# Performance work log

Hardware: AMD Instinct MI355X
Metric: run time of the kernel (lower is better)

The kernel has to match this reference:

```python
import jax, jax.numpy as jnp
import numpy as np

N, D, E, R = 1024, 128, 32768, 32  # nodes, hidden, edges, rank-net width
EPS = 1e-5


def setup_inputs() -> dict:
    key = jax.random.key(0)
    ks = jax.random.split(key, 16)
    s = 0.02
    f32 = jnp.float32
    return {
        "x": jax.random.normal(ks[0], (N, D), f32),
        "edge_index": jax.random.randint(ks[1], (2, E), 0, N),
        # SAGEConv (mean aggr): lin_l (with bias) on aggregated neighbors, lin_r (no bias) on root
        "W_l": jax.random.normal(ks[2], (D, D), f32) * s,
        "b_l": jnp.zeros((D,), f32),
        "W_r": jax.random.normal(ks[3], (D, D), f32) * s,
        # rank_net: Linear(D,32) -> ReLU -> Linear(32,1)
        "W1": jax.random.normal(ks[4], (R, D), f32) * s,
        "b1": jnp.zeros((R,), f32),
        "W2": jax.random.normal(ks[5], (1, R), f32) * s,
        "b2": jnp.zeros((1,), f32),
        # MambaBlock params
        "Wp": jax.random.normal(ks[6], (4 * D, D), f32) * s,   # proj, no bias
        "A": jax.random.normal(ks[7], (1, 1, D), f32) * s,
        "Bp": jax.random.normal(ks[8], (1, D, 1), f32) * s,
        "Dp": jnp.ones((1,), f32),
        "Wd": jax.random.normal(ks[9], (D, D), f32) * s,       # delta linear
        "bd": jnp.zeros((D,), f32),
    }


def reference(x, edge_index, W_l, b_l, W_r, W1, b1, W2, b2, Wp, A, Bp, Dp, Wd, bd):
    src, dst = edge_index[0], edge_index[1]

    # ---- SAGEConv (mean) + residual + GELU ----
    agg = jax.ops.segment_sum(x[src], dst, num_segments=N)                      # [N,D]
    cnt = jax.ops.segment_sum(jnp.ones((E,), x.dtype), dst, num_segments=N)    # [N]
    mean = agg / jnp.maximum(cnt, 1.0)[:, None]
    x_gnn = mean @ W_l.T + b_l + x @ W_r.T + x
    x_gnn = jax.nn.gelu(x_gnn, approximate=False)

    # ---- dynamic sort: rank_net score + degree, argsort descending ----
    scores = (jax.nn.relu(x_gnn @ W1.T + b1) @ W2.T + b2)[:, 0]                # [N]
    deg = jnp.zeros((N,), x.dtype).at[src].add(1.0).at[dst].add(1.0)
    scores = scores + deg
    idx = jnp.argsort(-scores)          # soft_rank is monotone -> same ordering as raw scores
    xs = x_gnn[idx]                      # [N,D]

    # ---- MambaBlock on the sorted node sequence (batch=1, seq_len=N, hidden=D) ----
    proj = xs @ Wp.T                                    # [N,4D]
    delta, _Bs, Cs, residual = jnp.split(proj, 4, axis=-1)  # split B is unused (as in source)
    delta = jax.nn.softplus(delta @ Wd.T + bd)          # [N,D]
    Av = A[0, 0]                                        # [D]
    Bv = Bp[0, :, 0]                                    # [D]
    dA = (jnp.exp(delta * Av) * Bv).T                   # [D,N]  einsum('blh,bhn->bhl') with n=1
    dB = jnp.cumsum(delta * Bv, axis=0).T               # [D,N]  cumsum over seq, n=1
    u = xs.T                                            # [D,N]
    Ct = Cs.T                                           # [D,N]
    kernel = jnp.einsum('hl,hn->hnl', dA, u) + dB[:, None, :]   # [D,N,N] large intermediate
    y = jnp.einsum('hnl,hn->hl', kernel, Ct).T                  # [N,D]
    out = y + residual * Dp[0]

    # F.layer_norm without affine params
    mu = out.mean(-1, keepdims=True)
    var = out.var(-1, keepdims=True)
    out = (out - mu) / jnp.sqrt(var + EPS)

    inv = jnp.argsort(idx)
    return x + out[inv]
```

## Files before the change

kernel.cpp:

```cpp
#include <hip/hip_runtime.h>

namespace {
constexpr int N   = 1024;
constexpr int D   = 128;
constexpr int E   = 32768;
constexpr int CAP = 128;

using short8  = __attribute__((ext_vector_type(8))) short;
using floatx4 = __attribute__((ext_vector_type(4))) float;

__device__ __forceinline__ unsigned short f2bf(float f){
  unsigned int u = __float_as_uint(f);
  unsigned int r = (u + 0x7FFFu + ((u >> 16) & 1u)) >> 16;
  return (unsigned short)r;
}
__device__ __forceinline__ float bf2f(unsigned short b){
  return __uint_as_float(((unsigned int)b) << 16);
}
__device__ __forceinline__ short8 ldfrag(const float* p){
  float4 a = *(const float4*)p;
  float4 b = *(const float4*)(p + 4);
  short8 r;
  r[0]=(short)f2bf(a.x); r[1]=(short)f2bf(a.y); r[2]=(short)f2bf(a.z); r[3]=(short)f2bf(a.w);
  r[4]=(short)f2bf(b.x); r[5]=(short)f2bf(b.y); r[6]=(short)f2bf(b.z); r[7]=(short)f2bf(b.w);
  return r;
}

__global__ __launch_bounds__(1024) void k_zero(int* __restrict__ cnt, int* __restrict__ srcdeg){
  int t = threadIdx.x;
  cnt[t] = 0;
  srcdeg[t] = 0;
}

__global__ void k_edges(const int* __restrict__ ei, int* __restrict__ cnt,
                        int* __restrict__ srcdeg, int* __restrict__ bucket){
  int e = blockIdx.x*256 + threadIdx.x;
  if(e < E){
    int s = ei[e], d = ei[E+e];
    int slot = atomicAdd(&cnt[d], 1);
    if(slot < CAP) bucket[d*CAP + slot] = s;
    atomicAdd(&srcdeg[s], 1);
  }
}

__global__ __launch_bounds__(256) void k_mean(const float* __restrict__ x,
    const int* __restrict__ cnt, const int* __restrict__ bucket,
    float* __restrict__ mean, float* __restrict__ s1, float* __restrict__ s2){
  int t = threadIdx.x;
  if(blockIdx.x == 0 && t < D){ s1[t] = 0.f; s2[t] = 0.f; }
  int f = t & 127, hh = t >> 7;
  int n = blockIdx.x*2 + hh;
  int c0 = cnt[n];
  int c = c0 < CAP ? c0 : CAP;
  const int* bk = bucket + n*CAP;
  float a0=0.f, a1=0.f, a2=0.f, a3=0.f;
  int j = 0;
  for(; j+3 < c; j += 4){
    int i0=bk[j], i1=bk[j+1], i2=bk[j+2], i3=bk[j+3];
    a0 += x[i0*D+f]; a1 += x[i1*D+f]; a2 += x[i2*D+f]; a3 += x[i3*D+f];
  }
  for(; j < c; ++j) a0 += x[bk[j]*D+f];
  mean[n*D + f] = (a0+a1+a2+a3) / (float)(c0 > 1 ? c0 : 1);
}


__global__ __launch_bounds__(64) void k_g1(
    const float* __restrict__ x, const float* __restrict__ mean,
    const float* __restrict__ Wl, const float* __restrict__ bl,
    const float* __restrict__ Wr, unsigned short* __restrict__ xg)
{
  int bid = blockIdx.x;
  int strip = bid >> 3, ct = bid & 7;
  int l = threadIdx.x, lr = l & 15, lg = l >> 4;
  int r0 = strip*16;

  const float* mrow = mean + (size_t)(r0+lr)*D + lg*8;
  const float* xrow = x    + (size_t)(r0+lr)*D + lg*8;
  short8 am[4], ax[4];
  #pragma unroll
  for(int s = 0; s < 4; ++s){ am[s] = ldfrag(mrow + s*32); ax[s] = ldfrag(xrow + s*32); }

  const float* wl = Wl + (size_t)(ct*16+lr)*D + lg*8;
  const float* wr = Wr + (size_t)(ct*16+lr)*D + lg*8;
  floatx4 acc = {0.f,0.f,0.f,0.f};
  #pragma unroll
  for(int s = 0; s < 4; ++s) acc = __builtin_amdgcn_mfma_f32_16x16x32_bf16(am[s], ldfrag(wl + s*32), acc, 0,0,0);
  #pragma unroll
  for(int s = 0; s < 4; ++s) acc = __builtin_amdgcn_mfma_f32_16x16x32_bf16(ax[s], ldfrag(wr + s*32), acc, 0,0,0);

  int col = ct*16 + lr;
  float blv = bl[col];
  #pragma unroll
  for(int rg = 0; rg < 4; ++rg){
    int row = lg*4 + rg;
    float v = acc[rg] + blv + x[(size_t)(r0+row)*D + col];
    float g = 0.5f*v*(1.0f + erff(v*0.7071067811865475f));
    xg[(size_t)(r0+row)*D + col] = f2bf(g);
  }
}

__global__ __launch_bounds__(64) void k_g2(
    const unsigned short* __restrict__ xg,
    const float* __restrict__ Wp, const float* __restrict__ W1,
    const float* __restrict__ b1, const float* __restrict__ W2,
    const float* __restrict__ b2,
    const int* __restrict__ cnt, const int* __restrict__ srcdeg,
    unsigned short* __restrict__ dr, float* __restrict__ res,
    float* __restrict__ s1, float* __restrict__ s2,
    float* __restrict__ scores)
{
  int bid = blockIdx.x;
  int strip = bid / 25, tt = bid - strip*25;
  int l = threadIdx.x, lr = l & 15, lg = l >> 4;
  int r0 = strip*16;

  const unsigned short* agp = xg + (size_t)(r0+lr)*D + lg*8;
  short8 ag[4];
  #pragma unroll
  for(int s = 0; s < 4; ++s) ag[s] = *(const short8*)(agp + s*32);

  if(tt < 24){
    int seg = tt >> 3, ctl = tt & 7;
    int wrow = (seg == 0) ? ctl*16 : (seg == 1) ? (2*D + ctl*16) : (3*D + ctl*16);
    const float* bp = Wp + (size_t)(wrow + lr)*D + lg*8;
    floatx4 acc = {0.f,0.f,0.f,0.f};
    #pragma unroll
    for(int s = 0; s < 4; ++s) acc = __builtin_amdgcn_mfma_f32_16x16x32_bf16(ag[s], ldfrag(bp + s*32), acc, 0,0,0);
    if(seg == 0){
      int col = ctl*16 + lr;
      #pragma unroll
      for(int rg = 0; rg < 4; ++rg) dr[(size_t)(r0+lg*4+rg)*D + col] = f2bf(acc[rg]);
    } else if(seg == 1){
      int h = ctl*16 + lr;
      float ls1 = 0.f, ls2 = 0.f;
      #pragma unroll
      for(int rg = 0; rg < 4; ++rg){
        float c = acc[rg];
        ls1 += bf2f(xg[(size_t)(r0+lg*4+rg)*D + h]) * c;
        ls2 += c;
      }
      ls1 += __shfl_xor(ls1, 16); ls1 += __shfl_xor(ls1, 32);
      ls2 += __shfl_xor(ls2, 16); ls2 += __shfl_xor(ls2, 32);
      if(lg == 0){ atomicAdd(&s1[h], ls1); atomicAdd(&s2[h], ls2); }
    } else {
      int col = ctl*16 + lr;
      #pragma unroll
      for(int rg = 0; rg < 4; ++rg) res[(size_t)(r0+lg*4+rg)*D + col] = acc[rg];
    }
  } else {
    floatx4 sa0 = {0.f,0.f,0.f,0.f}, sa1 = {0.f,0.f,0.f,0.f};
    const float* w10 = W1 + (size_t)(lr)*D + lg*8;
    const float* w11 = W1 + (size_t)(16+lr)*D + lg*8;
    #pragma unroll
    for(int s = 0; s < 4; ++s){
      sa0 = __builtin_amdgcn_mfma_f32_16x16x32_bf16(ag[s], ldfrag(w10 + s*32), sa0, 0,0,0);
      sa1 = __builtin_amdgcn_mfma_f32_16x16x32_bf16(ag[s], ldfrag(w11 + s*32), sa1, 0,0,0);
    }
    float b10 = b1[lr], b11 = b1[16+lr];
    float w20 = W2[lr], w21 = W2[16+lr];
    #pragma unroll
    for(int rg = 0; rg < 4; ++rg){
      float v = fmaxf(sa0[rg] + b10, 0.f)*w20 + fmaxf(sa1[rg] + b11, 0.f)*w21;
      v += __shfl_xor(v, 1); v += __shfl_xor(v, 2);
      v += __shfl_xor(v, 4); v += __shfl_xor(v, 8);
      if(lr == 0){
        int row = r0 + lg*4 + rg;
        scores[row] = v + b2[0] + (float)(cnt[row] + srcdeg[row]);
      }
    }
  }
}

__global__ __launch_bounds__(64) void k_g3rank(
    const unsigned short* __restrict__ dr,
    const float* __restrict__ Wd, const float* __restrict__ bd,
    float* __restrict__ delta,
    const float* __restrict__ scores, int* __restrict__ sidx)
{
  int bid = blockIdx.x;
  int l = threadIdx.x;
  if(bid < 512){
    int strip = bid >> 3, ct = bid & 7;
    int lr = l & 15, lg = l >> 4;
    int r0 = strip*16;
    const unsigned short* adp = dr + (size_t)(r0+lr)*D + lg*8;
    short8 ad[4];
    #pragma unroll
    for(int s = 0; s < 4; ++s) ad[s] = *(const short8*)(adp + s*32);
    const float* wd = Wd + (size_t)(ct*16+lr)*D + lg*8;
    floatx4 acc = {0.f,0.f,0.f,0.f};
    #pragma unroll
    for(int s = 0; s < 4; ++s) acc = __builtin_amdgcn_mfma_f32_16x16x32_bf16(ad[s], ldfrag(wd + s*32), acc, 0,0,0);
    int col = ct*16 + lr;
    float bdv = bd[col];
    #pragma unroll
    for(int rg = 0; rg < 4; ++rg){
      float d2 = acc[rg] + bdv;
      float sp = (d2 > 20.f) ? d2 : log1pf(expf(d2));
      delta[(size_t)(r0+lg*4+rg)*D + col] = sp;
    }
  } else {
    int i = bid - 512;
    float si = scores[i];
    int c = 0;
    #pragma unroll
    for(int ch = 0; ch < 4; ++ch){
      float4 sj = *(const float4*)&scores[l*4 + ch*256];
      #pragma unroll
      for(int k = 0; k < 4; ++k){
        int j = l*4 + ch*256 + k;
        float s = (k==0)?sj.x:(k==1)?sj.y:(k==2)?sj.z:sj.w;
        c += (s > si || (s == si && j < i)) ? 1 : 0;
      }
    }
    #pragma unroll
    for(int m = 1; m < 64; m <<= 1) c += __shfl_xor(c, m);
    if(l == 0) sidx[c] = i;
  }
}

__global__ __launch_bounds__(1024) void k_cumsum(const float* __restrict__ delta,
     const int* __restrict__ sidx, const float* __restrict__ Bp, float* __restrict__ pfx){
  int t = threadIdx.x, h0 = blockIdx.x*4;
  int i = sidx[t];
  float4 dv = *(const float4*)&delta[i*D + h0];
  float4 bv = *(const float4*)&Bp[h0];
  float v0 = dv.x*bv.x, v1 = dv.y*bv.y, v2 = dv.z*bv.z, v3 = dv.w*bv.w;
  int lane = t & 63, w = t >> 6;
  #pragma unroll
  for(int o2 = 1; o2 < 64; o2 <<= 1){
    float n0 = __shfl_up(v0, o2, 64), n1 = __shfl_up(v1, o2, 64);
    float n2 = __shfl_up(v2, o2, 64), n3 = __shfl_up(v3, o2, 64);
    if(lane >= o2){ v0 += n0; v1 += n1; v2 += n2; v3 += n3; }
  }
  __shared__ float4 wsum[16];
  if(lane == 63) wsum[w] = make_float4(v0, v1, v2, v3);
  __syncthreads();
  float p0=0.f, p1=0.f, p2=0.f, p3=0.f;
  #pragma unroll
  for(int i2 = 0; i2 < 16; ++i2){
    float4 sv = wsum[i2];
    if(i2 < w){ p0 += sv.x; p1 += sv.y; p2 += sv.z; p3 += sv.w; }
  }
  float4 outv; outv.x = v0+p0; outv.y = v1+p1; outv.z = v2+p2; outv.w = v3+p3;
  *(float4*)&pfx[t*D + h0] = outv;
}

__global__ __launch_bounds__(128) void k_final(
    const float* __restrict__ delta, const float* __restrict__ res,
    const float* __restrict__ pfx, const int* __restrict__ sidx,
    const float* __restrict__ s1, const float* __restrict__ s2,
    const float* __restrict__ A, const float* __restrict__ Bp,
    const float* __restrict__ Dp, const float* __restrict__ x,
    float* __restrict__ out){
  int l = blockIdx.x, h = threadIdx.x;
  int i = sidx[l];
  float dlt = delta[i*D + h];
  float dAv = expf(dlt * A[h]) * Bp[h];
  float o = dAv * s1[h] + pfx[l*D + h] * s2[h] + res[i*D + h] * Dp[0];
  __shared__ float sm1[2], sm2[2];
  float v = o;
  v += __shfl_down(v, 32); v += __shfl_down(v, 16); v += __shfl_down(v, 8);
  v += __shfl_down(v, 4);  v += __shfl_down(v, 2);  v += __shfl_down(v, 1);
  int wid = h >> 6, lane = h & 63;
  if(lane == 0) sm1[wid] = v;
  __syncthreads();
  float mean = (sm1[0] + sm1[1]) * (1.0f/(float)D);
  float cdev = o - mean;
  float cv = cdev * cdev;
  cv += __shfl_down(cv, 32); cv += __shfl_down(cv, 16); cv += __shfl_down(cv, 8);
  cv += __shfl_down(cv, 4);  cv += __shfl_down(cv, 2);  cv += __shfl_down(cv, 1);
  if(lane == 0) sm2[wid] = cv;
  __syncthreads();
  float var = (sm2[0] + sm2[1]) * (1.0f/(float)D);
  float nrm = cdev * rsqrtf(var + 1e-5f);
  out[i*D + h] = x[i*D + h] + nrm;
}

}

extern "C" void kernel_launch(void* const* d_in, const int* in_sizes, int n_in,
                              void* d_out, int out_size, void* d_ws, size_t ws_size,
                              hipStream_t stream){
  const float* x   = (const float*)d_in[0];
  const int*   ei  = (const int*)d_in[1];
  const float* Wl  = (const float*)d_in[2];
  const float* bl  = (const float*)d_in[3];
  const float* Wr  = (const float*)d_in[4];
  const float* W1  = (const float*)d_in[5];
  const float* b1  = (const float*)d_in[6];
  const float* W2  = (const float*)d_in[7];
  const float* b2  = (const float*)d_in[8];
  const float* Wp  = (const float*)d_in[9];
  const float* A   = (const float*)d_in[10];
  const float* Bp  = (const float*)d_in[11];
  const float* Dp  = (const float*)d_in[12];
  const float* Wd  = (const float*)d_in[13];
  const float* bd  = (const float*)d_in[14];

  char* ws = (char*)d_ws;
  size_t o = 0;
  auto alloc = [&](size_t bytes)->char*{
    char* p = ws + o;
    o = (o + bytes + 255) & ~(size_t)255;
    return p;
  };
  float* s1     = (float*)alloc(D*4);
  float* s2     = (float*)alloc(D*4);
  int*   cnt    = (int*)  alloc(N*4);
  int*   srcdeg = (int*)  alloc(N*4);
  int*   bucket = (int*)  alloc((size_t)N*CAP*4);
  float* meanb  = (float*)alloc((size_t)N*D*4);
  unsigned short* xg = (unsigned short*)alloc((size_t)N*D*2);
  unsigned short* dr = (unsigned short*)alloc((size_t)N*D*2);
  float* scores = (float*)alloc(N*4);
  int*   sidx   = (int*)  alloc(N*4);
  float* delta  = (float*)alloc((size_t)N*D*4);
  float* res    = (float*)alloc((size_t)N*D*4);
  float* pfx    = (float*)alloc((size_t)N*D*4);
  (void)ws_size; (void)in_sizes; (void)n_in; (void)out_size;

  k_zero  <<<1, 1024, 0, stream>>>(cnt, srcdeg);
  k_edges <<<(E+255)/256, 256, 0, stream>>>(ei, cnt, srcdeg, bucket);
  k_mean  <<<N/2, 256, 0, stream>>>(x, cnt, bucket, meanb, s1, s2);
  k_g1    <<<64*8, 64, 0, stream>>>(x, meanb, Wl, bl, Wr, xg);
  k_g2    <<<64*25, 64, 0, stream>>>(xg, Wp, W1, b1, W2, b2, cnt, srcdeg, dr, res, s1, s2, scores);
  k_g3rank<<<512+1024, 64, 0, stream>>>(dr, Wd, bd, delta, scores, sidx);
  k_cumsum<<<D/4, 1024, 0, stream>>>(delta, sidx, Bp, pfx);
  k_final <<<N, 128, 0, stream>>>(delta, res, pfx, sidx, s1, s2, A, Bp, Dp, x, (float*)d_out);
}
```

Before: 51.63 us.

## Pre-convert weights to bf16 once and split neighbor gather across two halves

The zero-init kernel now also converts Wl, Wr, Wd, W1 and Wp to bf16 buffers. The GEMM kernels load short8 fragments directly instead of loading fp32 and converting per tile, which removes repeated conversion work and halves weight bytes. The mean kernel now uses one block per node, with each half of the block summing half the neighbor list and the two partials combined through shared memory. This adds a conversion pass each call and a block sync in k_mean.

```diff
diff --git a/kernel.cpp b/kernel.cpp
--- a/kernel.cpp
+++ b/kernel.cpp
@@ -26,10 +26,32 @@
   return r;
 }
 
-__global__ __launch_bounds__(1024) void k_zero(int* __restrict__ cnt, int* __restrict__ srcdeg){
-  int t = threadIdx.x;
-  cnt[t] = 0;
-  srcdeg[t] = 0;
+__global__ __launch_bounds__(256) void k_zero(
+    int* __restrict__ cnt, int* __restrict__ srcdeg,
+    const float* __restrict__ Wl, const float* __restrict__ Wr,
+    const float* __restrict__ Wd, const float* __restrict__ W1,
+    const float* __restrict__ Wp,
+    unsigned short* __restrict__ wlb, unsigned short* __restrict__ wrb,
+    unsigned short* __restrict__ wdb, unsigned short* __restrict__ w1b,
+    unsigned short* __restrict__ wpb)
+{
+  int t = threadIdx.x, b = blockIdx.x;
+  if(b == 0){
+    ((int4*)cnt)[t]    = make_int4(0,0,0,0);
+    ((int4*)srcdeg)[t] = make_int4(0,0,0,0);
+    return;
+  }
+  const int T = 16384*3 + 4096 + 65536;
+  int stride = 128*256;
+  for(int i = (b-1)*256 + t; i < T; i += stride){
+    float v; unsigned short* dst;
+    if(i < 16384){            v = Wl[i];          dst = &wlb[i]; }
+    else if(i < 32768){       v = Wr[i-16384];    dst = &wrb[i-16384]; }
+    else if(i < 49152){       v = Wd[i-32768];    dst = &wdb[i-32768]; }
+    else if(i < 53248){       v = W1[i-49152];    dst = &w1b[i-49152]; }
+    else {                    v = Wp[i-53248];    dst = &wpb[i-53248]; }
+    *dst = f2bf(v);
+  }
 }
 
 __global__ void k_edges(const int* __restrict__ ei, int* __restrict__ cnt,
@@ -46,28 +68,34 @@
 __global__ __launch_bounds__(256) void k_mean(const float* __restrict__ x,
     const int* __restrict__ cnt, const int* __restrict__ bucket,
     float* __restrict__ mean, float* __restrict__ s1, float* __restrict__ s2){
+  __shared__ float sacc[128];
   int t = threadIdx.x;
-  if(blockIdx.x == 0 && t < D){ s1[t] = 0.f; s2[t] = 0.f; }
-  int f = t & 127, hh = t >> 7;
-  int n = blockIdx.x*2 + hh;
+  int n = blockIdx.x;
+  if(n == 0 && t < D){ s1[t] = 0.f; s2[t] = 0.f; }
+  int f = t & 127, j2 = t >> 7;
   int c0 = cnt[n];
   int c = c0 < CAP ? c0 : CAP;
   const int* bk = bucket + n*CAP;
+  int ch = (c + 1) >> 1;
+  int beg = j2 * ch, end = beg + ch < c ? beg + ch : c;
   float a0=0.f, a1=0.f, a2=0.f, a3=0.f;
-  int j = 0;
-  for(; j+3 < c; j += 4){
+  int j = beg;
+  for(; j+3 < end; j += 4){
     int i0=bk[j], i1=bk[j+1], i2=bk[j+2], i3=bk[j+3];
     a0 += x[i0*D+f]; a1 += x[i1*D+f]; a2 += x[i2*D+f]; a3 += x[i3*D+f];
   }
-  for(; j < c; ++j) a0 += x[bk[j]*D+f];
-  mean[n*D + f] = (a0+a1+a2+a3) / (float)(c0 > 1 ? c0 : 1);
+  for(; j < end; ++j) a0 += x[bk[j]*D+f];
+  float part = (a0+a1)+(a2+a3);
+  if(j2 == 1) sacc[f] = part;
+  __syncthreads();
+  if(j2 == 0) mean[n*D + f] = (part + sacc[f]) / (float)(c0 > 1 ? c0 : 1);
 }
 
 
 __global__ __launch_bounds__(64) void k_g1(
     const float* __restrict__ x, const float* __restrict__ mean,
-    const float* __restrict__ Wl, const float* __restrict__ bl,
-    const float* __restrict__ Wr, unsigned short* __restrict__ xg)
+    const unsigned short* __restrict__ wlb, const float* __restrict__ bl,
+    const unsigned short* __restrict__ wrb, unsigned short* __restrict__ xg)
 {
   int bid = blockIdx.x;
   int strip = bid >> 3, ct = bid & 7;
@@ -80,13 +108,13 @@
   #pragma unroll
   for(int s = 0; s < 4; ++s){ am[s] = ldfrag(mrow + s*32); ax[s] = ldfrag(xrow + s*32); }
 
-  const float* wl = Wl + (size_t)(ct*16+lr)*D + lg*8;
-  const float* wr = Wr + (size_t)(ct*16+lr)*D + lg*8;
+  const unsigned short* wl = wlb + (size_t)(ct*16+lr)*D + lg*8;
+  const unsigned short* wr = wrb + (size_t)(ct*16+lr)*D + lg*8;
   floatx4 acc = {0.f,0.f,0.f,0.f};
   #pragma unroll
-  for(int s = 0; s < 4; ++s) acc = __builtin_amdgcn_mfma_f32_16x16x32_bf16(am[s], ldfrag(wl + s*32), acc, 0,0,0);
-  #pragma unroll
-  for(int s = 0; s < 4; ++s) acc = __builtin_amdgcn_mfma_f32_16x16x32_bf16(ax[s], ldfrag(wr + s*32), acc, 0,0,0);
+  for(int s = 0; s < 4; ++s) acc = __builtin_amdgcn_mfma_f32_16x16x32_bf16(am[s], *(const short8*)(wl + s*32), acc, 0,0,0);
+  #pragma unroll
+  for(int s = 0; s < 4; ++s) acc = __builtin_amdgcn_mfma_f32_16x16x32_bf16(ax[s], *(const short8*)(wr + s*32), acc, 0,0,0);
 
   int col = ct*16 + lr;
   float blv = bl[col];
@@ -101,7 +129,7 @@
 
 __global__ __launch_bounds__(64) void k_g2(
     const unsigned short* __restrict__ xg,
-    const float* __restrict__ Wp, const float* __restrict__ W1,
+    const unsigned short* __restrict__ wpb, const unsigned short* __restrict__ w1b,
     const float* __restrict__ b1, const float* __restrict__ W2,
     const float* __restrict__ b2,
     const int* __restrict__ cnt, const int* __restrict__ srcdeg,
@@ -122,10 +150,10 @@
   if(tt < 24){
     int seg = tt >> 3, ctl = tt & 7;
     int wrow = (seg == 0) ? ctl*16 : (seg == 1) ? (2*D + ctl*16) : (3*D + ctl*16);
-    const float* bp = Wp + (size_t)(wrow + lr)*D + lg*8;
+    const unsigned short* bp = wpb + (size_t)(wrow + lr)*D + lg*8;
     floatx4 acc = {0.f,0.f,0.f,0.f};
     #pragma unroll
-    for(int s = 0; s < 4; ++s) acc = __builtin_amdgcn_mfma_f32_16x16x32_bf16(ag[s], ldfrag(bp + s*32), acc, 0,0,0);
+    for(int s = 0; s < 4; ++s) acc = __builtin_amdgcn_mfma_f32_16x16x32_bf16(ag[s], *(const short8*)(bp + s*32), acc, 0,0,0);
     if(seg == 0){
       int col = ctl*16 + lr;
       #pragma unroll
@@ -149,12 +177,12 @@
     }
   } else {
     floatx4 sa0 = {0.f,0.f,0.f,0.f}, sa1 = {0.f,0.f,0.f,0.f};
-    const float* w10 = W1 + (size_t)(lr)*D + lg*8;
-    const float* w11 = W1 + (size_t)(16+lr)*D + lg*8;
+    const unsigned short* w10 = w1b + (size_t)(lr)*D + lg*8;
+    const unsigned short* w11 = w1b + (size_t)(16+lr)*D + lg*8;
     #pragma unroll
     for(int s = 0; s < 4; ++s){
-      sa0 = __builtin_amdgcn_mfma_f32_16x16x32_bf16(ag[s], ldfrag(w10 + s*32), sa0, 0,0,0);
-      sa1 = __builtin_amdgcn_mfma_f32_16x16x32_bf16(ag[s], ldfrag(w11 + s*32), sa1, 0,0,0);
+      sa0 = __builtin_amdgcn_mfma_f32_16x16x32_bf16(ag[s], *(const short8*)(w10 + s*32), sa0, 0,0,0);
+      sa1 = __builtin_amdgcn_mfma_f32_16x16x32_bf16(ag[s], *(const short8*)(w11 + s*32), sa1, 0,0,0);
     }
     float b10 = b1[lr], b11 = b1[16+lr];
     float w20 = W2[lr], w21 = W2[16+lr];
@@ -173,7 +201,7 @@
 
 __global__ __launch_bounds__(64) void k_g3rank(
     const unsigned short* __restrict__ dr,
-    const float* __restrict__ Wd, const float* __restrict__ bd,
+    const unsigned short* __restrict__ wdb, const float* __restrict__ bd,
     float* __restrict__ delta,
     const float* __restrict__ scores, int* __restrict__ sidx)
 {
@@ -187,10 +215,10 @@
     short8 ad[4];
     #pragma unroll
     for(int s = 0; s < 4; ++s) ad[s] = *(const short8*)(adp + s*32);
-    const float* wd = Wd + (size_t)(ct*16+lr)*D + lg*8;
+    const unsigned short* wd = wdb + (size_t)(ct*16+lr)*D + lg*8;
     floatx4 acc = {0.f,0.f,0.f,0.f};
     #pragma unroll
-    for(int s = 0; s < 4; ++s) acc = __builtin_amdgcn_mfma_f32_16x16x32_bf16(ad[s], ldfrag(wd + s*32), acc, 0,0,0);
+    for(int s = 0; s < 4; ++s) acc = __builtin_amdgcn_mfma_f32_16x16x32_bf16(ad[s], *(const short8*)(wd + s*32), acc, 0,0,0);
     int col = ct*16 + lr;
     float bdv = bd[col];
     #pragma unroll
@@ -311,8 +339,13 @@
   int*   srcdeg = (int*)  alloc(N*4);
   int*   bucket = (int*)  alloc((size_t)N*CAP*4);
   float* meanb  = (float*)alloc((size_t)N*D*4);
-  unsigned short* xg = (unsigned short*)alloc((size_t)N*D*2);
-  unsigned short* dr = (unsigned short*)alloc((size_t)N*D*2);
+  unsigned short* xg  = (unsigned short*)alloc((size_t)N*D*2);
+  unsigned short* dr  = (unsigned short*)alloc((size_t)N*D*2);
+  unsigned short* wlb = (unsigned short*)alloc((size_t)D*D*2);
+  unsigned short* wrb = (unsigned short*)alloc((size_t)D*D*2);
+  unsigned short* wdb = (unsigned short*)alloc((size_t)D*D*2);
+  unsigned short* w1b = (unsigned short*)alloc((size_t)32*D*2);
+  unsigned short* wpb = (unsigned short*)alloc((size_t)4*D*D*2);
   float* scores = (float*)alloc(N*4);
   int*   sidx   = (int*)  alloc(N*4);
   float* delta  = (float*)alloc((size_t)N*D*4);
@@ -320,12 +353,12 @@
   float* pfx    = (float*)alloc((size_t)N*D*4);
   (void)ws_size; (void)in_sizes; (void)n_in; (void)out_size;
 
-  k_zero  <<<1, 1024, 0, stream>>>(cnt, srcdeg);
+  k_zero  <<<129, 256, 0, stream>>>(cnt, srcdeg, Wl, Wr, Wd, W1, Wp, wlb, wrb, wdb, w1b, wpb);
   k_edges <<<(E+255)/256, 256, 0, stream>>>(ei, cnt, srcdeg, bucket);
-  k_mean  <<<N/2, 256, 0, stream>>>(x, cnt, bucket, meanb, s1, s2);
-  k_g1    <<<64*8, 64, 0, stream>>>(x, meanb, Wl, bl, Wr, xg);
-  k_g2    <<<64*25, 64, 0, stream>>>(xg, Wp, W1, b1, W2, b2, cnt, srcdeg, dr, res, s1, s2, scores);
-  k_g3rank<<<512+1024, 64, 0, stream>>>(dr, Wd, bd, delta, scores, sidx);
+  k_mean  <<<N, 256, 0, stream>>>(x, cnt, bucket, meanb, s1, s2);
+  k_g1    <<<64*8, 64, 0, stream>>>(x, meanb, wlb, bl, wrb, xg);
+  k_g2    <<<64*25, 64, 0, stream>>>(xg, wpb, w1b, b1, W2, b2, cnt, srcdeg, dr, res, s1, s2, scores);
+  k_g3rank<<<512+1024, 64, 0, stream>>>(dr, wdb, bd, delta, scores, sidx);
   k_cumsum<<<D/4, 1024, 0, stream>>>(delta, sidx, Bp, pfx);
   k_final <<<N, 128, 0, stream>>>(delta, res, pfx, sidx, s1, s2, A, Bp, Dp, x, (float*)d_out);
 }
```

Result: faster. 49.50 us (-4.1%).
